# Performance work log

Measured on AMD Instinct MI355X. Metric: run time of the kernel, lower is better.

Reference implementation:

```python
import jax, jax.numpy as jnp
import numpy as np

EPS_AGG = 1e-6  # torch code adds 1e-6 to scatter weight sums
EPS_BN = 1e-5


def _pix_idx(loc_orig, H, W):
    # map normalized coords in [-1,1] to flat pixel index on an HxW grid
    loc = jnp.clip(loc_orig, -1.0, 1.0) * 0.5 + 0.5
    ix = jnp.round(loc[..., 0] * (W - 1)).astype(jnp.int32)
    iy = jnp.round(loc[..., 1] * (H - 1)).astype(jnp.int32)
    return iy * W + ix  # [B, N0]


def token2map(x, loc_orig, idx_agg, H, W):
    # scatter token features to a dense map, averaging collisions
    B, N, C = x.shape
    N0 = idx_agg.shape[1]
    idx_hw = _pix_idx(loc_orig, H, W)                                   # [B, N0]
    tok = jnp.take_along_axis(x, idx_agg[..., None], axis=1)            # [B, N0, C]
    flat = (idx_hw + jnp.arange(B, dtype=jnp.int32)[:, None] * (H * W)).reshape(-1)
    sums = jax.ops.segment_sum(tok.reshape(-1, C), flat, num_segments=B * H * W)
    cnt = jax.ops.segment_sum(jnp.ones((B * N0,), x.dtype), flat, num_segments=B * H * W)
    out = sums / (cnt[:, None] + EPS_AGG)
    return out.reshape(B, H, W, C).transpose(0, 3, 1, 2)                # [B, C, H, W]


def map2token(fmap, Nt, loc_orig, idx_agg_t, agg_weight_t):
    # gather map pixels back to Nt target tokens, weighted-averaging per token
    B, C, H, W = fmap.shape
    idx_hw = _pix_idx(loc_orig, H, W)                                   # [B, N0]
    pix = fmap.transpose(0, 2, 3, 1).reshape(B, H * W, C)
    gath = jnp.take_along_axis(pix, idx_hw[..., None], axis=1)          # [B, N0, C]
    flat = (idx_agg_t + jnp.arange(B, dtype=jnp.int32)[:, None] * Nt).reshape(-1)
    num = jax.ops.segment_sum((gath * agg_weight_t[..., None]).reshape(-1, C), flat, num_segments=B * Nt)
    den = jax.ops.segment_sum(agg_weight_t.reshape(-1), flat, num_segments=B * Nt)
    return (num / (den[:, None] + EPS_AGG)).reshape(B, Nt, C)


def token_downup(x, idx_agg_s, idx_agg_t, agg_weight_t, Nt):
    # weighted aggregation from N source tokens to Nt target tokens via N0 original positions
    B, N, C = x.shape
    src = jnp.take_along_axis(x, idx_agg_s[..., None], axis=1)          # [B, N0, C]
    flat = (idx_agg_t + jnp.arange(B, dtype=jnp.int32)[:, None] * Nt).reshape(-1)
    num = jax.ops.segment_sum((src * agg_weight_t[..., None]).reshape(-1, C), flat, num_segments=B * Nt)
    den = jax.ops.segment_sum(agg_weight_t.reshape(-1), flat, num_segments=B * Nt)
    return (num / (den[:, None] + EPS_AGG)).reshape(B, Nt, C)


def batchnorm(x, gamma, beta):
    # BatchNorm2d on [B,C,Nt,1] == per-channel stats over (B, Nt); x here is [B, Nt, C]
    mu = x.mean(axis=(0, 1), keepdims=True)
    var = x.var(axis=(0, 1), keepdims=True)
    return (x - mu) * jax.lax.rsqrt(var + EPS_BN) * gamma + beta


def setup_inputs() -> dict:
    key = jax.random.key(0)
    ks = jax.random.split(key, 12)
    B, N, N0, Nt, Cin, Cout, H, W = 32, 1568, 3136, 784, 256, 512, 56, 56
    x = jax.random.normal(ks[0], (B, N, Cin), dtype=jnp.float32)
    loc_orig = jax.random.uniform(ks[1], (B, N0, 2), dtype=jnp.float32, minval=-1.0, maxval=1.0)
    idx_agg = jax.random.randint(ks[2], (B, N0), 0, N, dtype=jnp.int32)
    agg_weight = jax.random.uniform(ks[3], (B, N0), dtype=jnp.float32)
    idx_agg_t = jax.random.randint(ks[4], (B, N0), 0, Nt, dtype=jnp.int32)
    agg_weight_t = jax.random.uniform(ks[5], (B, N0), dtype=jnp.float32)
    dw_w = jax.random.normal(ks[6], (Cin, 1, 3, 3), dtype=jnp.float32) * 0.1     # depthwise 3x3
    skip_w = jax.random.normal(ks[7], (Cin,), dtype=jnp.float32) * 0.1           # depthwise 1x1
    conv_w = jax.random.normal(ks[8], (Cout, Cin), dtype=jnp.float32) * (1.0 / np.sqrt(Cin))
    gamma1 = jnp.ones((Cin,), jnp.float32); beta1 = jnp.zeros((Cin,), jnp.float32)
    gamma2 = jnp.ones((Cout,), jnp.float32); beta2 = jnp.zeros((Cout,), jnp.float32)
    return {"x": x, "loc_orig": loc_orig, "idx_agg": idx_agg, "agg_weight": agg_weight,
            "idx_agg_t": idx_agg_t, "agg_weight_t": agg_weight_t, "H": H, "W": W, "Nt": Nt,
            "dw_w": dw_w, "skip_w": skip_w, "conv_w": conv_w,
            "gamma1": gamma1, "beta1": beta1, "gamma2": gamma2, "beta2": beta2}


def reference(x, loc_orig, idx_agg, agg_weight, idx_agg_t, agg_weight_t, H, W, Nt,
              dw_w, skip_w, conv_w, gamma1, beta1, gamma2, beta2):
    # token -> map scatter
    x_map = token2map(x, loc_orig, idx_agg, H, W)                       # [B, Cin, H, W]
    # 3x3 depthwise conv, stride 2, padding 1
    Cin = x_map.shape[1]
    x_map = jax.lax.conv_general_dilated(
        x_map, dw_w, window_strides=(2, 2), padding=((1, 1), (1, 1)),
        feature_group_count=Cin, dimension_numbers=("NCHW", "OIHW", "NCHW"))    # [B, Cin, H/2, W/2]
    # map -> target tokens gather
    x_back = map2token(x_map, Nt, loc_orig, idx_agg_t, agg_weight_t)    # [B, Nt, Cin]
    # skip path: token downsample + 1x1 depthwise (per-channel scale)
    xs = token_downup(x, idx_agg, idx_agg_t, agg_weight_t, Nt)          # [B, Nt, Cin]
    xs = xs * skip_w                                                    # dw_skip, groups=Cin, k=1
    y = xs + x_back
    y = batchnorm(y, gamma1, beta1)
    y = jnp.einsum("bnc,oc->bno", y, conv_w)                            # 1x1 conv Cin->Cout
    y = batchnorm(y, gamma2, beta2)
    return jax.nn.relu(y)                                               # [B, Nt, Cout]
```

## Files before the change

kernel.cpp:

```cpp
#include <hip/hip_runtime.h>

constexpr int B    = 32;
constexpr int N    = 1568;
constexpr int N0   = 3136;
constexpr int Nt   = 784;
constexpr int Cin  = 256;
constexpr int Cout = 512;
constexpr int H    = 56;
constexpr int W    = 56;
constexpr int HW   = 3136;
constexpr int Ho   = 28;
constexpr int Wo   = 28;
constexpr int HWo  = 784;
constexpr int RR   = B * Nt;
constexpr int NE   = B * N0;
constexpr int NBP  = B * HW;
constexpr int NBT  = B * Nt;
constexpr int NBO  = B * HWo;
constexpr int SB   = NBT + NBO;
constexpr int NCHUNK = SB / 256;

constexpr size_t W_HISTP = 0;
constexpr size_t W_HISTS = NBP;
constexpr size_t W_S1SUM = NBP + SB;
constexpr size_t W_S1SQ  = W_S1SUM + Cin;
constexpr size_t W_S2SUM = W_S1SQ + Cin;
constexpr size_t W_S2SQ  = W_S2SUM + Cout;
constexpr size_t W_OFF   = NBP + SB + 1536;
constexpr size_t W_CUR   = W_OFF + SB + 8;
constexpr size_t W_PC    = W_CUR + SB;
constexpr size_t W_BSUM  = W_PC + NE;
constexpr size_t W_LT    = W_BSUM + 512;
constexpr size_t W_LC    = W_LT + (size_t)2 * NE;
constexpr size_t W_CONVB = W_LC + (size_t)8 * NE;
constexpr size_t W_YBF   = W_CONVB + (size_t)B * HWo * Cin / 2;
constexpr size_t W_WFB   = W_YBF + (size_t)RR * Cin / 2;
constexpr size_t W_BIAS  = W_WFB + (size_t)Cout * Cin / 2;
constexpr size_t W_A2    = W_BIAS + Cout;
constexpr size_t W_C2    = W_A2 + Cout;
constexpr size_t W_ZB    = W_C2 + Cout;

__device__ __forceinline__ int pix_of(float t, float scale) {
    t = fminf(fmaxf(t, -1.0f), 1.0f);
    float u = __fadd_rn(__fmul_rn(t, 0.5f), 0.5f);
    return (int)rintf(__fmul_rn(u, scale));
}
__device__ __forceinline__ unsigned short f2bf(float f) {
    unsigned int u = __float_as_uint(f);
    u = (u + 0x7fffu + ((u >> 16) & 1u)) >> 16;
    return (unsigned short)u;
}
__device__ __forceinline__ float bf2f(unsigned short h) {
    return __uint_as_float(((unsigned int)h) << 16);
}

__global__ void k_hist(const float* __restrict__ loc, const int* __restrict__ idxt,
                       int* __restrict__ histP, int* __restrict__ histS,
                       int* __restrict__ pc) {
    int i = blockIdx.x * 256 + threadIdx.x;
    if (i >= NE) return;
    int b = i / N0;
    float lx = loc[(size_t)2 * i], ly = loc[(size_t)2 * i + 1];
    int ix = pix_of(lx, 55.0f), iy = pix_of(ly, 55.0f);
    int jx = pix_of(lx, 27.0f), jy = pix_of(ly, 27.0f);
    int p56 = iy * W + ix, p28 = jy * Wo + jx;
    pc[i] = p56 | (p28 << 16);
    atomicAdd(&histP[b * HW + p56], 1);
    atomicAdd(&histS[b * Nt + idxt[i]], 1);
    int oy_lo = iy >> 1, oy_hi = min(Ho - 1, (iy + 1) >> 1);
    int ox_lo = ix >> 1, ox_hi = min(Wo - 1, (ix + 1) >> 1);
    for (int oy = oy_lo; oy <= oy_hi; ++oy)
        for (int ox = ox_lo; ox <= ox_hi; ++ox)
            atomicAdd(&histS[NBT + b * HWo + oy * Wo + ox], 1);
}

__global__ void k_scanA(const int* __restrict__ hist, int* __restrict__ bsum) {
    __shared__ int sm[256];
    int i = blockIdx.x * 256 + threadIdx.x;
    sm[threadIdx.x] = hist[i];
    __syncthreads();
    for (int d = 128; d > 0; d >>= 1) {
        if (threadIdx.x < d) sm[threadIdx.x] += sm[threadIdx.x + d];
        __syncthreads();
    }
    if (threadIdx.x == 0) bsum[blockIdx.x] = sm[0];
}

__global__ void k_scanB(int* __restrict__ bsum) {
    __shared__ int sm[512];
    int t = threadIdx.x;
    int v = (t < NCHUNK) ? bsum[t] : 0;
    sm[t] = v; __syncthreads();
    for (int d = 1; d < 512; d <<= 1) {
        int u = (t >= d) ? sm[t - d] : 0;
        __syncthreads();
        sm[t] += u;
        __syncthreads();
    }
    if (t < NCHUNK) bsum[t] = sm[t] - v;
}

__global__ void k_scanC(const int* __restrict__ hist, const int* __restrict__ bsum,
                        int* __restrict__ off, int* __restrict__ cur) {
    __shared__ int sm[256];
    int t = threadIdx.x;
    int i = blockIdx.x * 256 + t;
    int v = hist[i];
    sm[t] = v; __syncthreads();
    for (int d = 1; d < 256; d <<= 1) {
        int u = (t >= d) ? sm[t - d] : 0;
        __syncthreads();
        sm[t] += u;
        __syncthreads();
    }
    int excl = bsum[blockIdx.x] + sm[t] - v;
    off[i] = excl; cur[i] = excl;
    if (i == SB - 1) off[SB] = excl + v;
}

__global__ void k_scat(const int* __restrict__ pc, const int* __restrict__ idxa,
                       const int* __restrict__ idxt, const float* __restrict__ wt,
                       const int* __restrict__ histP, int* __restrict__ cur,
                       int2* __restrict__ listT, int2* __restrict__ listC) {
    int i = blockIdx.x * 256 + threadIdx.x;
    if (i >= NE) return;
    int b = i / N0;
    int v = pc[i];
    int p56 = v & 0xFFFF, p28 = v >> 16;
    int s = idxa[i];
    int posT = atomicAdd(&cur[b * Nt + idxt[i]], 1);
    listT[posT] = make_int2(s | (p28 << 16), __float_as_int(wt[i]));
    float wrc = 1.0f / ((float)histP[b * HW + p56] + 1e-6f);
    int wrci = __float_as_int(wrc);
    int iy = p56 / W, ix = p56 - iy * W;
    int oy_lo = iy >> 1, oy_hi = min(Ho - 1, (iy + 1) >> 1);
    int ox_lo = ix >> 1, ox_hi = min(Wo - 1, (ix + 1) >> 1);
    for (int oy = oy_lo; oy <= oy_hi; ++oy)
        for (int ox = ox_lo; ox <= ox_hi; ++ox) {
            int tap = (iy - (2 * oy - 1)) * 3 + (ix - (2 * ox - 1));
            int posC = atomicAdd(&cur[NBT + b * HWo + oy * Wo + ox], 1) - NE;
            listC[posC] = make_int2(s | (tap << 16), wrci);
        }
}

__global__ __launch_bounds__(256) void k_gconv(const float* __restrict__ x,
        const int* __restrict__ off, const int2* __restrict__ listC,
        const float* __restrict__ dww, unsigned short* __restrict__ convb) {
    __shared__ float wsm[9 * 256];
    int blk = blockIdx.x, c = threadIdx.x;
    int b = blk / HWo;
#pragma unroll
    for (int k = 0; k < 9; ++k) wsm[k * 256 + c] = dww[c * 9 + k];
    int st = off[NBT + blk] - NE, en = off[NBT + blk + 1] - NE;
    __syncthreads();
    const float* xb = x + (size_t)b * N * Cin + c;
    float acc = 0.0f;
    int j = st;
    for (; j + 4 <= en; j += 4) {
        int2 e0 = listC[j], e1 = listC[j + 1], e2 = listC[j + 2], e3 = listC[j + 3];
        float v0 = xb[(size_t)(e0.x & 0xFFFF) * Cin];
        float v1 = xb[(size_t)(e1.x & 0xFFFF) * Cin];
        float v2 = xb[(size_t)(e2.x & 0xFFFF) * Cin];
        float v3 = xb[(size_t)(e3.x & 0xFFFF) * Cin];
        acc = fmaf(v0 * __int_as_float(e0.y), wsm[(e0.x >> 16) * 256 + c], acc);
        acc = fmaf(v1 * __int_as_float(e1.y), wsm[(e1.x >> 16) * 256 + c], acc);
        acc = fmaf(v2 * __int_as_float(e2.y), wsm[(e2.x >> 16) * 256 + c], acc);
        acc = fmaf(v3 * __int_as_float(e3.y), wsm[(e3.x >> 16) * 256 + c], acc);
    }
    for (; j < en; ++j) {
        int2 e = listC[j];
        acc = fmaf(xb[(size_t)(e.x & 0xFFFF) * Cin] * __int_as_float(e.y),
                   wsm[(e.x >> 16) * 256 + c], acc);
    }
    convb[(size_t)blk * Cin + c] = f2bf(acc);
}

__global__ __launch_bounds__(256) void k_gtok(const float* __restrict__ x,
        const unsigned short* __restrict__ convb, const int* __restrict__ off,
        const int2* __restrict__ listT, const float* __restrict__ skipw,
        unsigned short* __restrict__ ybf) {
    int bt = blockIdx.x, c = threadIdx.x;
    int b = bt / Nt;
    int st = off[bt], en = off[bt + 1];
    float sk = skipw[c];
    const float* xb = x + (size_t)b * N * Cin + c;
    const unsigned short* cb = convb + (size_t)b * HWo * Cin + c;
    float acc = 0.0f, wsum = 0.0f;
    int j = st;
    for (; j + 2 <= en; j += 2) {
        int2 e0 = listT[j], e1 = listT[j + 1];
        float w0 = __int_as_float(e0.y), w1 = __int_as_float(e1.y);
        float cv0 = bf2f(cb[(size_t)(e0.x >> 16) * Cin]);
        float cv1 = bf2f(cb[(size_t)(e1.x >> 16) * Cin]);
        float xv0 = xb[(size_t)(e0.x & 0xFFFF) * Cin];
        float xv1 = xb[(size_t)(e1.x & 0xFFFF) * Cin];
        wsum += w0 + w1;
        acc = fmaf(w0, cv0 + sk * xv0, acc);
        acc = fmaf(w1, cv1 + sk * xv1, acc);
    }
    for (; j < en; ++j) {
        int2 e = listT[j];
        float w = __int_as_float(e.y);
        wsum += w;
        float cv = bf2f(cb[(size_t)(e.x >> 16) * Cin]);
        acc = fmaf(w, cv + sk * xb[(size_t)(e.x & 0xFFFF) * Cin], acc);
    }
    ybf[(size_t)bt * Cin + c] = f2bf(acc * (1.0f / (wsum + 1e-6f)));
}

__global__ void k_ystats(const unsigned short* __restrict__ ybf,
                         float* __restrict__ s1, float* __restrict__ s1q) {
    int c = threadIdx.x;
    float sum = 0.0f, sq = 0.0f;
    for (int r = blockIdx.x; r < RR; r += gridDim.x) {
        float v = bf2f(ybf[(size_t)r * Cin + c]);
        sum += v;
        sq = fmaf(v, v, sq);
    }
    atomicAdd(&s1[c], sum);
    atomicAdd(&s1q[c], sq);
}

__global__ void k_fold(const float* __restrict__ s1, const float* __restrict__ s1q,
                       const float* __restrict__ g1, const float* __restrict__ b1,
                       const float* __restrict__ convw, unsigned short* __restrict__ wfb,
                       float* __restrict__ bias) {
    int o = blockIdx.x, c = threadIdx.x;
    const float inv = 1.0f / (float)RR;
    float mu  = s1[c] * inv;
    float var = s1q[c] * inv - mu * mu;
    float a   = g1[c] / sqrtf(var + 1e-5f);
    float bs  = b1[c] - mu * a;
    float wv  = convw[(size_t)o * Cin + c];
    wfb[(size_t)o * Cin + c] = f2bf(wv * a);
    __shared__ float red[256];
    red[c] = wv * bs;
    __syncthreads();
    for (int st = 128; st > 0; st >>= 1) {
        if (c < st) red[c] += red[c + st];
        __syncthreads();
    }
    if (c == 0) bias[o] = red[0];
}

typedef __attribute__((ext_vector_type(8))) short short8;
typedef __attribute__((ext_vector_type(4))) float f32x4;

__global__ __launch_bounds__(256) void k_gemm(const unsigned short* __restrict__ A,
        const unsigned short* __restrict__ Bt, const float* __restrict__ bias,
        unsigned short* __restrict__ zb, float* __restrict__ s2, float* __restrict__ s2q) {
    constexpr int BK = 32, LS = 48;
    __shared__ unsigned short As[128 * LS];
    __shared__ unsigned short Bs[128 * LS];
    __shared__ float rsum[128], rsq[128];
    int m0 = blockIdx.x * 128, n0 = blockIdx.y * 128;
    int t = threadIdx.x;
    int wave = t >> 6, lane = t & 63;
    int wm = wave >> 1, wn = wave & 1;
    int l16 = lane & 15, lq = lane >> 4;
    f32x4 acc[4][4];
#pragma unroll
    for (int i = 0; i < 4; ++i)
#pragma unroll
        for (int j = 0; j < 4; ++j) acc[i][j] = (f32x4)0.0f;
    if (t < 128) { rsum[t] = 0.0f; rsq[t] = 0.0f; }

    for (int k0 = 0; k0 < Cin; k0 += BK) {
#pragma unroll
        for (int r2 = 0; r2 < 2; ++r2) {
            int e = r2 * 256 + t;
            int row = e >> 2, kc = (e & 3) * 8;
            *(float4*)&As[row * LS + kc] = *(const float4*)&A[((size_t)(m0 + row)) * Cin + k0 + kc];
            *(float4*)&Bs[row * LS + kc] = *(const float4*)&Bt[((size_t)(n0 + row)) * Cin + k0 + kc];
        }
        __syncthreads();
        short8 af[4], bf[4];
#pragma unroll
        for (int i = 0; i < 4; ++i) {
            af[i] = *(short8*)&As[(wm * 64 + i * 16 + l16) * LS + lq * 8];
            bf[i] = *(short8*)&Bs[(wn * 64 + i * 16 + l16) * LS + lq * 8];
        }
#pragma unroll
        for (int i = 0; i < 4; ++i)
#pragma unroll
            for (int j = 0; j < 4; ++j)
                acc[i][j] = __builtin_amdgcn_mfma_f32_16x16x32_bf16(af[i], bf[j], acc[i][j], 0, 0, 0);
        __syncthreads();
    }
#pragma unroll
    for (int j = 0; j < 4; ++j) {
        int cl  = wn * 64 + j * 16 + l16;
        int col = n0 + cl;
        float bv = bias[col];
        float ps = 0.0f, pq = 0.0f;
#pragma unroll
        for (int i = 0; i < 4; ++i) {
            int rbase = m0 + wm * 64 + i * 16 + lq * 4;
#pragma unroll
            for (int r = 0; r < 4; ++r) {
                float v = acc[i][j][r] + bv;
                zb[(size_t)(rbase + r) * Cout + col] = f2bf(v);
                ps += v;
                pq = fmaf(v, v, pq);
            }
        }
        atomicAdd(&rsum[cl], ps);
        atomicAdd(&rsq[cl], pq);
    }
    __syncthreads();
    if (t < 128) {
        atomicAdd(&s2[n0 + t], rsum[t]);
        atomicAdd(&s2q[n0 + t], rsq[t]);
    }
}

__global__ void k_fold2(const float* __restrict__ s2, const float* __restrict__ s2q,
                        const float* __restrict__ g2, const float* __restrict__ b2,
                        float* __restrict__ a2, float* __restrict__ c2) {
    int o = threadIdx.x;
    const float inv = 1.0f / (float)RR;
    float mu  = s2[o] * inv;
    float var = s2q[o] * inv - mu * mu;
    float a   = g2[o] / sqrtf(var + 1e-5f);
    a2[o] = a;
    c2[o] = b2[o] - mu * a;
}

__global__ void k_final(const unsigned short* __restrict__ zb, const float* __restrict__ a2,
                        const float* __restrict__ c2, float* __restrict__ out) {
    size_t j4 = ((size_t)blockIdx.x * 256 + threadIdx.x) * 4;
    int o = (int)(j4 & (Cout - 1));
    uint2 u = *(const uint2*)&zb[j4];
    float e0 = bf2f((unsigned short)(u.x & 0xffffu));
    float e1 = bf2f((unsigned short)(u.x >> 16));
    float e2 = bf2f((unsigned short)(u.y & 0xffffu));
    float e3 = bf2f((unsigned short)(u.y >> 16));
    float4 r;
    r.x = fmaxf(fmaf(e0, a2[o + 0], c2[o + 0]), 0.0f);
    r.y = fmaxf(fmaf(e1, a2[o + 1], c2[o + 1]), 0.0f);
    r.z = fmaxf(fmaf(e2, a2[o + 2], c2[o + 2]), 0.0f);
    r.w = fmaxf(fmaf(e3, a2[o + 3], c2[o + 3]), 0.0f);
    *(float4*)&out[j4] = r;
}

extern "C" void kernel_launch(void* const* d_in, const int* in_sizes, int n_in,
                              void* d_out, int out_size, void* d_ws, size_t ws_size,
                              hipStream_t stream) {
    const float* x     = (const float*)d_in[0];
    const float* loc   = (const float*)d_in[1];
    const int*   idxa  = (const int*)d_in[2];
    const int*   idxt  = (const int*)d_in[4];
    const float* wt    = (const float*)d_in[5];
    const float* dww   = (const float*)d_in[9];
    const float* skipw = (const float*)d_in[10];
    const float* convw = (const float*)d_in[11];
    const float* g1    = (const float*)d_in[12];
    const float* b1    = (const float*)d_in[13];
    const float* g2    = (const float*)d_in[14];
    const float* b2    = (const float*)d_in[15];

    float* ws = (float*)d_ws;
    int*   histP = (int*)(ws + W_HISTP);
    int*   histS = (int*)(ws + W_HISTS);
    float* s1sum = ws + W_S1SUM;
    float* s1sq  = ws + W_S1SQ;
    float* s2sum = ws + W_S2SUM;
    float* s2sq  = ws + W_S2SQ;
    int*   off   = (int*)(ws + W_OFF);
    int*   cur   = (int*)(ws + W_CUR);
    int*   pc    = (int*)(ws + W_PC);
    int*   bsum  = (int*)(ws + W_BSUM);
    int2*  listT = (int2*)(ws + W_LT);
    int2*  listC = (int2*)(ws + W_LC);
    unsigned short* convb = (unsigned short*)(ws + W_CONVB);
    unsigned short* ybf   = (unsigned short*)(ws + W_YBF);
    unsigned short* wfb   = (unsigned short*)(ws + W_WFB);
    float* bias  = ws + W_BIAS;
    float* a2    = ws + W_A2;
    float* c2    = ws + W_C2;
    unsigned short* zb = (unsigned short*)(ws + W_ZB);
    float* out   = (float*)d_out;

    hipMemsetAsync(histP, 0, (size_t)(NBP + SB + 1536) * sizeof(float), stream);

    k_hist<<<NE / 256, 256, 0, stream>>>(loc, idxt, histP, histS, pc);
    k_scanA<<<NCHUNK, 256, 0, stream>>>(histS, bsum);
    k_scanB<<<1, 512, 0, stream>>>(bsum);
    k_scanC<<<NCHUNK, 256, 0, stream>>>(histS, bsum, off, cur);
    k_scat<<<NE / 256, 256, 0, stream>>>(pc, idxa, idxt, wt, histP, cur, listT, listC);

    k_gconv<<<NBO, 256, 0, stream>>>(x, off, listC, dww, convb);
    k_gtok<<<NBT, 256, 0, stream>>>(x, convb, off, listT, skipw, ybf);
    k_ystats<<<256, 256, 0, stream>>>(ybf, s1sum, s1sq);
    k_fold<<<Cout, 256, 0, stream>>>(s1sum, s1sq, g1, b1, convw, wfb, bias);

    dim3 gg(RR / 128, Cout / 128);
    k_gemm<<<gg, 256, 0, stream>>>(ybf, wfb, bias, zb, s2sum, s2sq);
    k_fold2<<<1, 512, 0, stream>>>(s2sum, s2sq, g2, b2, a2, c2);
    k_final<<<(int)(((size_t)RR * Cout) / 1024), 256, 0, stream>>>(zb, a2, c2, out);
}
```

Measured before the change: 300.7 us.

## Map one wavefront per output row with float4 gathers; fold BN2 stats into final

The gather-conv and gather-token kernels now give each 64-lane wavefront one output pixel or token and each lane four channels. Loads become float4 and uint2 vectors, stores are packed bf16, and segment bounds are kept uniform with readfirstlane. Blocks now cover four rows each, cutting block count and per-thread scalar loads. k_ystats reads two bf16 channels per thread, and the separate fold2 kernel is removed by recomputing BN2 scale and shift inside k_final, which adds per-element redundant rsqrt work.

```diff
diff --git a/kernel.cpp b/kernel.cpp
--- a/kernel.cpp
+++ b/kernel.cpp
@@ -36,9 +36,7 @@
 constexpr size_t W_YBF   = W_CONVB + (size_t)B * HWo * Cin / 2;
 constexpr size_t W_WFB   = W_YBF + (size_t)RR * Cin / 2;
 constexpr size_t W_BIAS  = W_WFB + (size_t)Cout * Cin / 2;
-constexpr size_t W_A2    = W_BIAS + Cout;
-constexpr size_t W_C2    = W_A2 + Cout;
-constexpr size_t W_ZB    = W_C2 + Cout;
+constexpr size_t W_ZB    = W_BIAS + Cout;
 
 __device__ __forceinline__ int pix_of(float t, float scale) {
     t = fminf(fmaxf(t, -1.0f), 1.0f);
@@ -147,78 +145,129 @@
         const int* __restrict__ off, const int2* __restrict__ listC,
         const float* __restrict__ dww, unsigned short* __restrict__ convb) {
     __shared__ float wsm[9 * 256];
-    int blk = blockIdx.x, c = threadIdx.x;
-    int b = blk / HWo;
-#pragma unroll
-    for (int k = 0; k < 9; ++k) wsm[k * 256 + c] = dww[c * 9 + k];
-    int st = off[NBT + blk] - NE, en = off[NBT + blk + 1] - NE;
+    int t = threadIdx.x;
+#pragma unroll
+    for (int k = 0; k < 9; ++k) wsm[k * 256 + t] = dww[t * 9 + k];
+    int wv = t >> 6, lane = t & 63;
+    int blk = blockIdx.x * 4 + wv;
+    int b   = __builtin_amdgcn_readfirstlane(blk / HWo);
+    int st  = __builtin_amdgcn_readfirstlane(off[NBT + blk]) - NE;
+    int en  = __builtin_amdgcn_readfirstlane(off[NBT + blk + 1]) - NE;
     __syncthreads();
-    const float* xb = x + (size_t)b * N * Cin + c;
-    float acc = 0.0f;
+    const float* xb = x + (size_t)b * N * Cin;
+    float4 acc = make_float4(0.f, 0.f, 0.f, 0.f);
     int j = st;
     for (; j + 4 <= en; j += 4) {
         int2 e0 = listC[j], e1 = listC[j + 1], e2 = listC[j + 2], e3 = listC[j + 3];
-        float v0 = xb[(size_t)(e0.x & 0xFFFF) * Cin];
-        float v1 = xb[(size_t)(e1.x & 0xFFFF) * Cin];
-        float v2 = xb[(size_t)(e2.x & 0xFFFF) * Cin];
-        float v3 = xb[(size_t)(e3.x & 0xFFFF) * Cin];
-        acc = fmaf(v0 * __int_as_float(e0.y), wsm[(e0.x >> 16) * 256 + c], acc);
-        acc = fmaf(v1 * __int_as_float(e1.y), wsm[(e1.x >> 16) * 256 + c], acc);
-        acc = fmaf(v2 * __int_as_float(e2.y), wsm[(e2.x >> 16) * 256 + c], acc);
-        acc = fmaf(v3 * __int_as_float(e3.y), wsm[(e3.x >> 16) * 256 + c], acc);
+        float4 v0 = ((const float4*)(xb + (size_t)(e0.x & 0xFFFF) * Cin))[lane];
+        float4 v1 = ((const float4*)(xb + (size_t)(e1.x & 0xFFFF) * Cin))[lane];
+        float4 v2 = ((const float4*)(xb + (size_t)(e2.x & 0xFFFF) * Cin))[lane];
+        float4 v3 = ((const float4*)(xb + (size_t)(e3.x & 0xFFFF) * Cin))[lane];
+        float4 w0 = *(const float4*)&wsm[(e0.x >> 16) * 256 + lane * 4];
+        float4 w1 = *(const float4*)&wsm[(e1.x >> 16) * 256 + lane * 4];
+        float4 w2 = *(const float4*)&wsm[(e2.x >> 16) * 256 + lane * 4];
+        float4 w3 = *(const float4*)&wsm[(e3.x >> 16) * 256 + lane * 4];
+        float r0 = __int_as_float(e0.y), r1 = __int_as_float(e1.y);
+        float r2 = __int_as_float(e2.y), r3 = __int_as_float(e3.y);
+        acc.x = fmaf(v0.x * r0, w0.x, acc.x);
+        acc.y = fmaf(v0.y * r0, w0.y, acc.y);
+        acc.z = fmaf(v0.z * r0, w0.z, acc.z);
+        acc.w = fmaf(v0.w * r0, w0.w, acc.w);
+        acc.x = fmaf(v1.x * r1, w1.x, acc.x);
+        acc.y = fmaf(v1.y * r1, w1.y, acc.y);
+        acc.z = fmaf(v1.z * r1, w1.z, acc.z);
+        acc.w = fmaf(v1.w * r1, w1.w, acc.w);
+        acc.x = fmaf(v2.x * r2, w2.x, acc.x);
+        acc.y = fmaf(v2.y * r2, w2.y, acc.y);
+        acc.z = fmaf(v2.z * r2, w2.z, acc.z);
+        acc.w = fmaf(v2.w * r2, w2.w, acc.w);
+        acc.x = fmaf(v3.x * r3, w3.x, acc.x);
+        acc.y = fmaf(v3.y * r3, w3.y, acc.y);
+        acc.z = fmaf(v3.z * r3, w3.z, acc.z);
+        acc.w = fmaf(v3.w * r3, w3.w, acc.w);
     }
     for (; j < en; ++j) {
         int2 e = listC[j];
-        acc = fmaf(xb[(size_t)(e.x & 0xFFFF) * Cin] * __int_as_float(e.y),
-                   wsm[(e.x >> 16) * 256 + c], acc);
-    }
-    convb[(size_t)blk * Cin + c] = f2bf(acc);
+        float4 v = ((const float4*)(xb + (size_t)(e.x & 0xFFFF) * Cin))[lane];
+        float4 wq = *(const float4*)&wsm[(e.x >> 16) * 256 + lane * 4];
+        float r = __int_as_float(e.y);
+        acc.x = fmaf(v.x * r, wq.x, acc.x);
+        acc.y = fmaf(v.y * r, wq.y, acc.y);
+        acc.z = fmaf(v.z * r, wq.z, acc.z);
+        acc.w = fmaf(v.w * r, wq.w, acc.w);
+    }
+    uint2 o;
+    o.x = (unsigned int)f2bf(acc.x) | ((unsigned int)f2bf(acc.y) << 16);
+    o.y = (unsigned int)f2bf(acc.z) | ((unsigned int)f2bf(acc.w) << 16);
+    ((uint2*)(convb + (size_t)blk * Cin))[lane] = o;
 }
 
 __global__ __launch_bounds__(256) void k_gtok(const float* __restrict__ x,
         const unsigned short* __restrict__ convb, const int* __restrict__ off,
         const int2* __restrict__ listT, const float* __restrict__ skipw,
         unsigned short* __restrict__ ybf) {
-    int bt = blockIdx.x, c = threadIdx.x;
-    int b = bt / Nt;
-    int st = off[bt], en = off[bt + 1];
-    float sk = skipw[c];
-    const float* xb = x + (size_t)b * N * Cin + c;
-    const unsigned short* cb = convb + (size_t)b * HWo * Cin + c;
-    float acc = 0.0f, wsum = 0.0f;
+    int t = threadIdx.x, wv = t >> 6, lane = t & 63;
+    int bt = blockIdx.x * 4 + wv;
+    int b  = __builtin_amdgcn_readfirstlane(bt / Nt);
+    int st = __builtin_amdgcn_readfirstlane(off[bt]);
+    int en = __builtin_amdgcn_readfirstlane(off[bt + 1]);
+    const float* xb = x + (size_t)b * N * Cin;
+    const unsigned short* cbb = convb + (size_t)b * HWo * Cin;
+    float4 sk = ((const float4*)skipw)[lane];
+    float4 acc = make_float4(0.f, 0.f, 0.f, 0.f);
+    float wsum = 0.0f;
     int j = st;
     for (; j + 2 <= en; j += 2) {
         int2 e0 = listT[j], e1 = listT[j + 1];
+        float4 xv0 = ((const float4*)(xb + (size_t)(e0.x & 0xFFFF) * Cin))[lane];
+        float4 xv1 = ((const float4*)(xb + (size_t)(e1.x & 0xFFFF) * Cin))[lane];
+        uint2 cv0 = ((const uint2*)(cbb + (size_t)(e0.x >> 16) * Cin))[lane];
+        uint2 cv1 = ((const uint2*)(cbb + (size_t)(e1.x >> 16) * Cin))[lane];
         float w0 = __int_as_float(e0.y), w1 = __int_as_float(e1.y);
-        float cv0 = bf2f(cb[(size_t)(e0.x >> 16) * Cin]);
-        float cv1 = bf2f(cb[(size_t)(e1.x >> 16) * Cin]);
-        float xv0 = xb[(size_t)(e0.x & 0xFFFF) * Cin];
-        float xv1 = xb[(size_t)(e1.x & 0xFFFF) * Cin];
         wsum += w0 + w1;
-        acc = fmaf(w0, cv0 + sk * xv0, acc);
-        acc = fmaf(w1, cv1 + sk * xv1, acc);
+        acc.x = fmaf(w0, bf2f((unsigned short)(cv0.x & 0xffffu)) + sk.x * xv0.x, acc.x);
+        acc.y = fmaf(w0, bf2f((unsigned short)(cv0.x >> 16))     + sk.y * xv0.y, acc.y);
+        acc.z = fmaf(w0, bf2f((unsigned short)(cv0.y & 0xffffu)) + sk.z * xv0.z, acc.z);
+        acc.w = fmaf(w0, bf2f((unsigned short)(cv0.y >> 16))     + sk.w * xv0.w, acc.w);
+        acc.x = fmaf(w1, bf2f((unsigned short)(cv1.x & 0xffffu)) + sk.x * xv1.x, acc.x);
+        acc.y = fmaf(w1, bf2f((unsigned short)(cv1.x >> 16))     + sk.y * xv1.y, acc.y);
+        acc.z = fmaf(w1, bf2f((unsigned short)(cv1.y & 0xffffu)) + sk.z * xv1.z, acc.z);
+        acc.w = fmaf(w1, bf2f((unsigned short)(cv1.y >> 16))     + sk.w * xv1.w, acc.w);
     }
     for (; j < en; ++j) {
         int2 e = listT[j];
+        float4 xv = ((const float4*)(xb + (size_t)(e.x & 0xFFFF) * Cin))[lane];
+        uint2 cv = ((const uint2*)(cbb + (size_t)(e.x >> 16) * Cin))[lane];
         float w = __int_as_float(e.y);
         wsum += w;
-        float cv = bf2f(cb[(size_t)(e.x >> 16) * Cin]);
-        acc = fmaf(w, cv + sk * xb[(size_t)(e.x & 0xFFFF) * Cin], acc);
-    }
-    ybf[(size_t)bt * Cin + c] = f2bf(acc * (1.0f / (wsum + 1e-6f)));
+        acc.x = fmaf(w, bf2f((unsigned short)(cv.x & 0xffffu)) + sk.x * xv.x, acc.x);
+        acc.y = fmaf(w, bf2f((unsigned short)(cv.x >> 16))     + sk.y * xv.y, acc.y);
+        acc.z = fmaf(w, bf2f((unsigned short)(cv.y & 0xffffu)) + sk.z * xv.z, acc.z);
+        acc.w = fmaf(w, bf2f((unsigned short)(cv.y >> 16))     + sk.w * xv.w, acc.w);
+    }
+    float rw = 1.0f / (wsum + 1e-6f);
+    uint2 o;
+    o.x = (unsigned int)f2bf(acc.x * rw) | ((unsigned int)f2bf(acc.y * rw) << 16);
+    o.y = (unsigned int)f2bf(acc.z * rw) | ((unsigned int)f2bf(acc.w * rw) << 16);
+    ((uint2*)(ybf + (size_t)bt * Cin))[lane] = o;
 }
 
 __global__ void k_ystats(const unsigned short* __restrict__ ybf,
                          float* __restrict__ s1, float* __restrict__ s1q) {
-    int c = threadIdx.x;
-    float sum = 0.0f, sq = 0.0f;
-    for (int r = blockIdx.x; r < RR; r += gridDim.x) {
-        float v = bf2f(ybf[(size_t)r * Cin + c]);
-        sum += v;
-        sq = fmaf(v, v, sq);
-    }
-    atomicAdd(&s1[c], sum);
-    atomicAdd(&s1q[c], sq);
+    int t = threadIdx.x;
+    int half = t >> 7, ci = t & 127;
+    float sum0 = 0.f, sq0 = 0.f, sum1 = 0.f, sq1 = 0.f;
+    for (int r = blockIdx.x * 2 + half; r < RR; r += gridDim.x * 2) {
+        unsigned int u = ((const unsigned int*)(ybf + (size_t)r * Cin))[ci];
+        float v0 = bf2f((unsigned short)(u & 0xffffu));
+        float v1 = bf2f((unsigned short)(u >> 16));
+        sum0 += v0; sq0 = fmaf(v0, v0, sq0);
+        sum1 += v1; sq1 = fmaf(v1, v1, sq1);
+    }
+    atomicAdd(&s1[ci * 2],      sum0);
+    atomicAdd(&s1q[ci * 2],     sq0);
+    atomicAdd(&s1[ci * 2 + 1],  sum1);
+    atomicAdd(&s1q[ci * 2 + 1], sq1);
 }
 
 __global__ void k_fold(const float* __restrict__ s1, const float* __restrict__ s1q,
@@ -314,32 +363,31 @@
     }
 }
 
-__global__ void k_fold2(const float* __restrict__ s2, const float* __restrict__ s2q,
+__global__ void k_final(const unsigned short* __restrict__ zb,
+                        const float* __restrict__ s2, const float* __restrict__ s2q,
                         const float* __restrict__ g2, const float* __restrict__ b2,
-                        float* __restrict__ a2, float* __restrict__ c2) {
-    int o = threadIdx.x;
-    const float inv = 1.0f / (float)RR;
-    float mu  = s2[o] * inv;
-    float var = s2q[o] * inv - mu * mu;
-    float a   = g2[o] / sqrtf(var + 1e-5f);
-    a2[o] = a;
-    c2[o] = b2[o] - mu * a;
-}
-
-__global__ void k_final(const unsigned short* __restrict__ zb, const float* __restrict__ a2,
-                        const float* __restrict__ c2, float* __restrict__ out) {
+                        float* __restrict__ out) {
     size_t j4 = ((size_t)blockIdx.x * 256 + threadIdx.x) * 4;
     int o = (int)(j4 & (Cout - 1));
+    const float inv = 1.0f / (float)RR;
     uint2 u = *(const uint2*)&zb[j4];
     float e0 = bf2f((unsigned short)(u.x & 0xffffu));
     float e1 = bf2f((unsigned short)(u.x >> 16));
     float e2 = bf2f((unsigned short)(u.y & 0xffffu));
     float e3 = bf2f((unsigned short)(u.y >> 16));
+    float mu0 = s2[o + 0] * inv, a0 = g2[o + 0] * rsqrtf(s2q[o + 0] * inv - mu0 * mu0 + 1e-5f);
+    float mu1 = s2[o + 1] * inv, a1 = g2[o + 1] * rsqrtf(s2q[o + 1] * inv - mu1 * mu1 + 1e-5f);
+    float mu2 = s2[o + 2] * inv, a2 = g2[o + 2] * rsqrtf(s2q[o + 2] * inv - mu2 * mu2 + 1e-5f);
+    float mu3 = s2[o + 3] * inv, a3 = g2[o + 3] * rsqrtf(s2q[o + 3] * inv - mu3 * mu3 + 1e-5f);
+    float c0 = b2[o + 0] - mu0 * a0;
+    float c1 = b2[o + 1] - mu1 * a1;
+    float c2 = b2[o + 2] - mu2 * a2;
+    float c3 = b2[o + 3] - mu3 * a3;
     float4 r;
-    r.x = fmaxf(fmaf(e0, a2[o + 0], c2[o + 0]), 0.0f);
-    r.y = fmaxf(fmaf(e1, a2[o + 1], c2[o + 1]), 0.0f);
-    r.z = fmaxf(fmaf(e2, a2[o + 2], c2[o + 2]), 0.0f);
-    r.w = fmaxf(fmaf(e3, a2[o + 3], c2[o + 3]), 0.0f);
+    r.x = fmaxf(fmaf(e0, a0, c0), 0.0f);
+    r.y = fmaxf(fmaf(e1, a1, c1), 0.0f);
+    r.z = fmaxf(fmaf(e2, a2, c2), 0.0f);
+    r.w = fmaxf(fmaf(e3, a3, c3), 0.0f);
     *(float4*)&out[j4] = r;
 }
 
@@ -376,8 +424,6 @@
     unsigned short* ybf   = (unsigned short*)(ws + W_YBF);
     unsigned short* wfb   = (unsigned short*)(ws + W_WFB);
     float* bias  = ws + W_BIAS;
-    float* a2    = ws + W_A2;
-    float* c2    = ws + W_C2;
     unsigned short* zb = (unsigned short*)(ws + W_ZB);
     float* out   = (float*)d_out;
 
@@ -389,13 +435,12 @@
     k_scanC<<<NCHUNK, 256, 0, stream>>>(histS, bsum, off, cur);
     k_scat<<<NE / 256, 256, 0, stream>>>(pc, idxa, idxt, wt, histP, cur, listT, listC);
 
-    k_gconv<<<NBO, 256, 0, stream>>>(x, off, listC, dww, convb);
-    k_gtok<<<NBT, 256, 0, stream>>>(x, convb, off, listT, skipw, ybf);
+    k_gconv<<<NBO / 4, 256, 0, stream>>>(x, off, listC, dww, convb);
+    k_gtok<<<NBT / 4, 256, 0, stream>>>(x, convb, off, listT, skipw, ybf);
     k_ystats<<<256, 256, 0, stream>>>(ybf, s1sum, s1sq);
     k_fold<<<Cout, 256, 0, stream>>>(s1sum, s1sq, g1, b1, convw, wfb, bias);
 
     dim3 gg(RR / 128, Cout / 128);
     k_gemm<<<gg, 256, 0, stream>>>(ybf, wfb, bias, zb, s2sum, s2sq);
-    k_fold2<<<1, 512, 0, stream>>>(s2sum, s2sq, g2, b2, a2, c2);
-    k_final<<<(int)(((size_t)RR * Cout) / 1024), 256, 0, stream>>>(zb, a2, c2, out);
-}
+    k_final<<<(int)(((size_t)RR * Cout) / 1024), 256, 0, stream>>>(zb, s2sum, s2sq, g2, b2, out);
+}
```

Measured after the change: 287.7 us. 4.3% less time.
